# Optimization experiments

Measured on AMD Instinct MI355X. Metric: run time of the kernel, lower is better.

The kernel has to match this reference:

```python
import jax, jax.numpy as jnp
import numpy as np

B, S, E = 4, 2048, 1024
H = 16
D = E // H  # head_dim = 64


def setup_inputs() -> dict:
    key = jax.random.key(0)
    k1, k2, k3 = jax.random.split(key, 3)
    scale_qkv = 1.0 / np.sqrt(E)
    return {
        "x": jax.random.normal(k1, (B, S, E), dtype=jnp.float32),
        "Wqkv": jax.random.normal(k2, (E, 3 * E), dtype=jnp.float32) * scale_qkv,
        "bqkv": jnp.zeros((3 * E,), dtype=jnp.float32),
        "Wproj": jax.random.normal(k3, (E, E), dtype=jnp.float32) * scale_qkv,
        "bproj": jnp.zeros((E,), dtype=jnp.float32),
    }


def reference(x, Wqkv, bqkv, Wproj, bproj):
    b, s, e = x.shape
    qkv = x @ Wqkv + bqkv                      # [B,S,3E]
    q, k, v = jnp.split(qkv, 3, axis=-1)
    # [B,S,E] -> [B,H,S,D]
    q = q.reshape(b, s, H, D).transpose(0, 2, 1, 3)
    k = k.reshape(b, s, H, D).transpose(0, 2, 1, 3)
    v = v.reshape(b, s, H, D).transpose(0, 2, 1, 3)
    scores = jnp.einsum('bhqd,bhkd->bhqk', q, k) * (D ** -0.5)  # [B,H,S,S]
    causal = jnp.tril(jnp.ones((s, s), dtype=bool))
    scores = jnp.where(causal, scores, -jnp.inf)
    weights = jax.nn.softmax(scores, axis=-1)  # dropout p=0 -> identity
    out = jnp.einsum('bhqk,bhkd->bhqd', weights, v)  # [B,H,S,D]
    out = out.transpose(0, 2, 1, 3).reshape(b, s, e)
    return out @ Wproj + bproj
```

## Files before the change

kernel.cpp:

```cpp
#include <hip/hip_runtime.h>
#include <hip/hip_bf16.h>
#include <stdint.h>

#define B_ 4
#define S_ 2048
#define E_ 1024
#define H_ 16
#define D_ 64
#define M_ 8192
#define N1_ 3072
#define QSCALE 0.18033688011112042f

typedef __attribute__((ext_vector_type(8))) short bf16x8;
typedef __attribute__((ext_vector_type(4))) float f32x4;
typedef __attribute__((ext_vector_type(16))) float f32x16;
typedef __attribute__((ext_vector_type(4))) short short4v;

__device__ __forceinline__ short f2b(float f) {
  union { float f; unsigned u; } c; c.f = f;
  unsigned u = c.u + 0x7fffu + ((c.u >> 16) & 1u);
  return (short)(u >> 16);
}

__device__ __forceinline__ float fexp2(float x) {
#if __has_builtin(__builtin_amdgcn_exp2f)
  return __builtin_amdgcn_exp2f(x);
#else
  return exp2f(x);
#endif
}

__device__ __forceinline__ unsigned cvtpk(float lo, float hi2) {
  unsigned r;
  asm("v_cvt_pk_bf16_f32 %0, %1, %2" : "=v"(r) : "v"(lo), "v"(hi2));
  return r;
}

__device__ __forceinline__ void gload16(const void* g, void* l) {
  __builtin_amdgcn_global_load_lds((const __attribute__((address_space(1))) void*)g,
                                   (__attribute__((address_space(3))) void*)l, 16, 0, 0);
}

__global__ void conv_kernel(const float* __restrict__ in, short* __restrict__ out) {
  int idx = blockIdx.x * 256 + threadIdx.x;
  const float4* p = (const float4*)in;
  float4 a = p[(size_t)idx * 2];
  float4 b = p[(size_t)idx * 2 + 1];
  bf16x8 v;
  v[0] = f2b(a.x); v[1] = f2b(a.y); v[2] = f2b(a.z); v[3] = f2b(a.w);
  v[4] = f2b(b.x); v[5] = f2b(b.y); v[6] = f2b(b.z); v[7] = f2b(b.w);
  *(bf16x8*)(out + (size_t)idx * 8) = v;
}

__global__ void trans_kernel(const float* __restrict__ in, short* __restrict__ out,
                             int K, int N) {
  __shared__ float tile[32][33];
  int n0 = blockIdx.x * 32, k0 = blockIdx.y * 32;
  int tx = threadIdx.x & 31, ty = threadIdx.x >> 5;
  #pragma unroll
  for (int i = 0; i < 4; ++i)
    tile[ty + i * 8][tx] = in[(size_t)(k0 + ty + i * 8) * N + n0 + tx];
  __syncthreads();
  #pragma unroll
  for (int i = 0; i < 4; ++i)
    out[(size_t)(n0 + ty + i * 8) * K + k0 + tx] = f2b(tile[tx][ty + i * 8]);
}

template<bool SCATTER>
__global__ __launch_bounds__(256)
void gemm_kernel(const short* __restrict__ A, const short* __restrict__ Bt,
                 const float* __restrict__ bias,
                 short* __restrict__ oQ, short* __restrict__ oK, short* __restrict__ oV,
                 float* __restrict__ oC, int Kdim, int Ndim)
{
  __shared__ short Asub[128 * 64];
  __shared__ short Bsub[128 * 64];
  const int tid = threadIdx.x;
  const int l = tid & 63, w = tid >> 6;
  const int wr = w >> 1, wc = w & 1;
  const int lr = l & 15, lg = l >> 4;

  const int nwg = gridDim.x * gridDim.y;
  const int lin = blockIdx.y * gridDim.x + blockIdx.x;
  const int lin2 = (lin & 7) * (nwg >> 3) + (lin >> 3);
  const int m0 = (lin2 / gridDim.x) * 128, n0 = (lin2 % gridDim.x) * 128;

  const int srow = w * 8 + (l >> 3);
  const int scol = ((l & 7) ^ (l >> 3)) << 3;

  f32x4 acc[4][4] = {};

  for (int k0 = 0; k0 < Kdim; k0 += 64) {
    __syncthreads();
    #pragma unroll
    for (int i = 0; i < 4; ++i) {
      gload16(A  + (size_t)(m0 + i * 32 + srow) * Kdim + k0 + scol,
              (char*)Asub + (i * 32 + w * 8) * 128);
      gload16(Bt + (size_t)(n0 + i * 32 + srow) * Kdim + k0 + scol,
              (char*)Bsub + (i * 32 + w * 8) * 128);
    }
    __syncthreads();
    #pragma unroll
    for (int kk = 0; kk < 64; kk += 32) {
      bf16x8 af[4], bfr[4];
      const int ce2 = (kk + lg * 8) << 1;
      #pragma unroll
      for (int mi = 0; mi < 4; ++mi) {
        int rr = wr * 64 + mi * 16 + lr;
        af[mi] = *(const bf16x8*)((const char*)Asub + rr * 128 + (ce2 ^ ((rr & 7) << 4)));
      }
      #pragma unroll
      for (int ni = 0; ni < 4; ++ni) {
        int rr = wc * 64 + ni * 16 + lr;
        bfr[ni] = *(const bf16x8*)((const char*)Bsub + rr * 128 + (ce2 ^ ((rr & 7) << 4)));
      }
      __builtin_amdgcn_s_setprio(1);
      #pragma unroll
      for (int mi = 0; mi < 4; ++mi)
        #pragma unroll
        for (int ni = 0; ni < 4; ++ni)
          acc[mi][ni] = __builtin_amdgcn_mfma_f32_16x16x32_bf16(af[mi], bfr[ni], acc[mi][ni], 0, 0, 0);
      __builtin_amdgcn_s_setprio(0);
    }
  }

  #pragma unroll
  for (int mi = 0; mi < 4; ++mi) {
    #pragma unroll
    for (int ni = 0; ni < 4; ++ni) {
      const int row0 = m0 + wr * 64 + mi * 16 + lg * 4;
      const int col  = n0 + wc * 64 + ni * 16 + lr;
      const float bv = bias[col];
      if constexpr (SCATTER) {
        const int which = col >> 10;
        const int e = col & 1023;
        const int h = e >> 6, d = e & 63;
        const int b = row0 >> 11, s = row0 & 2047;
        if (which == 2) {
          short4v pv;
          #pragma unroll
          for (int r = 0; r < 4; ++r) pv[r] = f2b(acc[mi][ni][r] + bv);
          *(short4v*)(oV + ((size_t)((b * H_ + h) * D_ + d)) * S_ + s) = pv;
        } else {
          short* dst = which ? oK : oQ;
          const float sc = which ? 1.0f : QSCALE;
          #pragma unroll
          for (int r = 0; r < 4; ++r)
            dst[((size_t)((b * H_ + h) * S_ + s + r)) * D_ + d] = f2b((acc[mi][ni][r] + bv) * sc);
        }
      } else {
        #pragma unroll
        for (int r = 0; r < 4; ++r)
          oC[(size_t)(row0 + r) * Ndim + col] = acc[mi][ni][r] + bv;
      }
    }
  }
}

__global__ __launch_bounds__(512)
void attn_kernel(const short* __restrict__ Q, const short* __restrict__ K,
                 const short* __restrict__ vT, short* __restrict__ O)
{
  __shared__ short Kl[4][64 * 64];
  __shared__ short Vl[4][64 * 64];

  const int qt = (S_ / 128 - 1) - (blockIdx.x >> 6);
  const int bh = blockIdx.x & 63;
  const int tid = threadIdx.x, l = tid & 63, w = tid >> 6;
  const int qw = w & 3, g = w >> 2;
  const int lc = l & 31, hi = l >> 5;
  const int sl8 = l >> 3;
  const int scol = 8 * ((l & 7) ^ sl8);

  const short* Qb = Q  + (size_t)bh * (S_ * D_);
  const short* Kb = K  + (size_t)bh * (S_ * D_);
  const short* Vg = vT + (size_t)bh * (S_ * D_);

  const int q0w = qt * 128 + qw * 32;
  const int ktL = (q0w + 31) >> 6;
  const int NT2 = qt + 1;

  bf16x8 qr[4];
  #pragma unroll
  for (int ds = 0; ds < 4; ++ds)
    qr[ds] = *(const bf16x8*)(Qb + (size_t)(q0w + lc) * D_ + ds * 16 + hi * 8);

  f32x16 accA{}, accB{};
  float lsum = 0.f;

  auto stage = [&](int slot, int kt2) {
    short* kl = &Kl[slot][(qw * 8) * 64];
    short* vl = &Vl[slot][(qw * 8) * 64];
    const size_t kr = (size_t)(kt2 * 64 + qw * 8 + sl8);
    gload16(Kb + kr * 64 + scol, kl);
    gload16(Kb + (kr + 32) * 64 + scol, kl + 32 * 64);
    const size_t vr = (size_t)(qw * 8 + sl8);
    gload16(Vg + vr * S_ + kt2 * 64 + scol, vl);
    gload16(Vg + (vr + 32) * S_ + kt2 * 64 + scol, vl + 32 * 64);
  };

  stage(g * 2, g);
  __syncthreads();

  for (int i = 0; i < NT2; ++i) {
    const int kt = 2 * i + g;
    const int slot = g * 2 + (i & 1);
    if (i + 1 < NT2) stage(g * 2 + ((i & 1) ^ 1), kt + 2);

    if (kt <= ktL) {
      const char* Kc = (const char*)Kl[slot];
      const char* Vc = (const char*)Vl[slot];
      const int rsw = (lc & 7) << 4;
      f32x16 s0{}, s1{};
      __builtin_amdgcn_s_setprio(1);
      #pragma unroll
      for (int ds = 0; ds < 4; ++ds) {
        const int byt = ds * 32 + hi * 16;
        bf16x8 a0 = *(const bf16x8*)(Kc + lc * 128 + (byt ^ rsw));
        bf16x8 a1 = *(const bf16x8*)(Kc + (32 + lc) * 128 + (byt ^ rsw));
        s0 = __builtin_amdgcn_mfma_f32_32x32x16_bf16(a0, qr[ds], s0, 0, 0, 0);
        s1 = __builtin_amdgcn_mfma_f32_32x32x16_bf16(a1, qr[ds], s1, 0, 0, 0);
      }
      __builtin_amdgcn_s_setprio(0);
      float p[32];
      #pragma unroll
      for (int r = 0; r < 16; ++r) { p[r] = s0[r]; p[16 + r] = s1[r]; }
      if (kt == ktL) {
        const int qq = q0w + lc - kt * 64;
        #pragma unroll
        for (int r = 0; r < 16; ++r) {
          const int k0 = (r & 3) + 8 * (r >> 2) + 4 * hi;
          if (k0 > qq)      p[r]      = -1e30f;
          if (k0 + 32 > qq) p[16 + r] = -1e30f;
        }
      }
      float rs0 = 0.f, rs1 = 0.f, rs2 = 0.f, rs3 = 0.f;
      #pragma unroll
      for (int r = 0; r < 8; ++r) {
        p[r]      = fexp2(p[r]);      rs0 += p[r];
        p[8 + r]  = fexp2(p[8 + r]);  rs1 += p[8 + r];
        p[16 + r] = fexp2(p[16 + r]); rs2 += p[16 + r];
        p[24 + r] = fexp2(p[24 + r]); rs3 += p[24 + r];
      }
      float rs = (rs0 + rs1) + (rs2 + rs3);
      rs += __shfl_xor(rs, 32);
      lsum += rs;
      #pragma unroll
      for (int ks = 0; ks < 4; ++ks) {
        const int b8 = ks * 8;
        const unsigned A0 = cvtpk(p[b8 + 0], p[b8 + 1]);
        const unsigned A1 = cvtpk(p[b8 + 2], p[b8 + 3]);
        const unsigned B0 = cvtpk(p[b8 + 4], p[b8 + 5]);
        const unsigned B1 = cvtpk(p[b8 + 6], p[b8 + 7]);
        const unsigned u0 = __shfl_xor(hi ? A0 : B0, 32);
        const unsigned u1 = __shfl_xor(hi ? A1 : B1, 32);
        union { unsigned u[4]; bf16x8 v; } W;
        W.u[0] = hi ? u0 : A0;
        W.u[1] = hi ? u1 : A1;
        W.u[2] = hi ? B0 : u0;
        W.u[3] = hi ? B1 : u1;
        const int byt = ks * 32 + hi * 16;
        bf16x8 va = *(const bf16x8*)(Vc + lc * 128 + (byt ^ rsw));
        bf16x8 vb = *(const bf16x8*)(Vc + (32 + lc) * 128 + (byt ^ rsw));
        __builtin_amdgcn_s_setprio(1);
        accA = __builtin_amdgcn_mfma_f32_32x32x16_bf16(va, W.v, accA, 0, 0, 0);
        accB = __builtin_amdgcn_mfma_f32_32x32x16_bf16(vb, W.v, accB, 0, 0, 0);
        __builtin_amdgcn_s_setprio(0);
      }
    }
    __syncthreads();
  }

  float* accsA = (float*)Kl;
  float* accsB = (float*)Vl;
  float* stats = (float*)((char*)Kl + 20480);
  const int mi = qw * 64 + l;
  if (g == 1) {
    #pragma unroll
    for (int r = 0; r < 16; ++r) {
      accsA[mi * 17 + r] = accA[r];
      accsB[mi * 17 + r] = accB[r];
    }
    stats[mi] = lsum;
  }
  __syncthreads();
  if (g == 0) {
    const float rl = 1.0f / (lsum + stats[mi]);
    const int h = bh & 15, b = bh >> 4;
    short* Ob = O + ((size_t)(b * S_ + q0w + lc)) * E_ + h * 64;
    #pragma unroll
    for (int gq = 0; gq < 4; ++gq) {
      short4v o0, o1;
      #pragma unroll
      for (int i = 0; i < 4; ++i) {
        o0[i] = f2b((accA[4 * gq + i] + accsA[mi * 17 + 4 * gq + i]) * rl);
        o1[i] = f2b((accB[4 * gq + i] + accsB[mi * 17 + 4 * gq + i]) * rl);
      }
      *(short4v*)(Ob + 8 * gq + 4 * hi) = o0;
      *(short4v*)(Ob + 32 + 8 * gq + 4 * hi) = o1;
    }
  }
}

extern "C" void kernel_launch(void* const* d_in, const int* in_sizes, int n_in,
                              void* d_out, int out_size, void* d_ws, size_t ws_size,
                              hipStream_t stream)
{
  const float* x     = (const float*)d_in[0];
  const float* Wqkv  = (const float*)d_in[1];
  const float* bqkv  = (const float*)d_in[2];
  const float* Wproj = (const float*)d_in[3];
  const float* bproj = (const float*)d_in[4];
  float* out = (float*)d_out;

  char* ws = (char*)d_ws;
  short* xb     = (short*)(ws + (size_t)0);
  short* wqkvT  = (short*)(ws + (size_t)16 * 1024 * 1024);
  short* wprojT = (short*)(ws + (size_t)22 * 1024 * 1024);
  short* qb     = (short*)(ws + (size_t)24 * 1024 * 1024);
  short* kb     = (short*)(ws + (size_t)40 * 1024 * 1024);
  short* vb     = (short*)(ws + (size_t)56 * 1024 * 1024);
  short* ob     = (short*)(ws + (size_t)72 * 1024 * 1024);

  conv_kernel<<<4096, 256, 0, stream>>>(x, xb);
  trans_kernel<<<dim3(N1_ / 32, E_ / 32), 256, 0, stream>>>(Wqkv, wqkvT, E_, N1_);
  trans_kernel<<<dim3(E_ / 32, E_ / 32), 256, 0, stream>>>(Wproj, wprojT, E_, E_);
  gemm_kernel<true><<<dim3(N1_ / 128, M_ / 128), 256, 0, stream>>>(
      xb, wqkvT, bqkv, qb, kb, vb, nullptr, E_, N1_);
  attn_kernel<<<(S_ / 128) * (B_ * H_), 512, 0, stream>>>(qb, kb, vb, ob);
  gemm_kernel<false><<<dim3(E_ / 128, M_ / 128), 256, 0, stream>>>(
      ob, wprojT, bproj, nullptr, nullptr, nullptr, out, E_, E_);
}
```

Before: 165.6 us.

## Use 256x128 GEMM tiles with triple-buffered async LDS prefetch

Both GEMM launches now use 512-thread blocks that compute 256x128 output tiles, with each wave owning a 128x32 slab. A three-stage LDS ring filled by async global-to-LDS loads prefetches two K-steps ahead, and a vmcnt wait plus a single barrier per iteration replace the two syncthreads. The goal is to overlap global loads with MFMA work and raise arithmetic intensity per block. In exchange the kernel needs 144KB of dynamic LDS, so only one block fits per CU, and the grid is halved, which may leave CUs underfilled on the smaller projection GEMM.

```diff
diff --git a/kernel.cpp b/kernel.cpp
--- a/kernel.cpp
+++ b/kernel.cpp
@@ -67,69 +67,95 @@
 }
 
 template<bool SCATTER>
-__global__ __launch_bounds__(256)
+__global__ __launch_bounds__(512)
 void gemm_kernel(const short* __restrict__ A, const short* __restrict__ Bt,
                  const float* __restrict__ bias,
                  short* __restrict__ oQ, short* __restrict__ oK, short* __restrict__ oV,
                  float* __restrict__ oC, int Kdim, int Ndim)
 {
-  __shared__ short Asub[128 * 64];
-  __shared__ short Bsub[128 * 64];
+  extern __shared__ char smem[];
+  char* Ab = smem;
+  char* Bb = smem + 3 * 32768;
+
   const int tid = threadIdx.x;
   const int l = tid & 63, w = tid >> 6;
-  const int wr = w >> 1, wc = w & 1;
+  const int wr = w >> 2, wc = w & 3;
   const int lr = l & 15, lg = l >> 4;
 
   const int nwg = gridDim.x * gridDim.y;
   const int lin = blockIdx.y * gridDim.x + blockIdx.x;
   const int lin2 = (lin & 7) * (nwg >> 3) + (lin >> 3);
-  const int m0 = (lin2 / gridDim.x) * 128, n0 = (lin2 % gridDim.x) * 128;
-
-  const int srow = w * 8 + (l >> 3);
-  const int scol = ((l & 7) ^ (l >> 3)) << 3;
-
-  f32x4 acc[4][4] = {};
-
-  for (int k0 = 0; k0 < Kdim; k0 += 64) {
-    __syncthreads();
-    #pragma unroll
-    for (int i = 0; i < 4; ++i) {
-      gload16(A  + (size_t)(m0 + i * 32 + srow) * Kdim + k0 + scol,
-              (char*)Asub + (i * 32 + w * 8) * 128);
-      gload16(Bt + (size_t)(n0 + i * 32 + srow) * Kdim + k0 + scol,
-              (char*)Bsub + (i * 32 + w * 8) * 128);
-    }
-    __syncthreads();
+  const int m0 = (lin2 / gridDim.x) * 256, n0 = (lin2 % gridDim.x) * 128;
+
+  const int srow = tid >> 3;
+  const int scol = 8 * ((tid & 7) ^ (srow & 7));
+  const int NT = Kdim >> 6;
+
+  f32x4 acc[8][2] = {};
+
+  #define STAGE_A(buf, t, chunk) \
+    gload16(A + (size_t)(m0 + (chunk) * 64 + srow) * Kdim + (t) * 64 + scol, \
+            Ab + (buf) * 32768 + (chunk) * 8192 + tid * 16)
+  #define STAGE_B(buf, t, chunk) \
+    gload16(Bt + (size_t)(n0 + (chunk) * 64 + srow) * Kdim + (t) * 64 + scol, \
+            Bb + (buf) * 16384 + (chunk) * 8192 + tid * 16)
+
+  STAGE_A(0, 0, 0); STAGE_A(0, 0, 1); STAGE_A(0, 0, 2); STAGE_A(0, 0, 3);
+  STAGE_B(0, 0, 0); STAGE_B(0, 0, 1);
+  if (NT > 1) {
+    STAGE_A(1, 1, 0); STAGE_A(1, 1, 1); STAGE_A(1, 1, 2); STAGE_A(1, 1, 3);
+    STAGE_B(1, 1, 0); STAGE_B(1, 1, 1);
+  }
+
+  int buf = 0;
+  for (int t = 0; t < NT; ++t) {
+    if (t + 1 < NT) asm volatile("s_waitcnt vmcnt(6)" ::: "memory");
+    else            asm volatile("s_waitcnt vmcnt(0)" ::: "memory");
+    __builtin_amdgcn_s_barrier();
+    asm volatile("" ::: "memory");
+
+    const char* Ac = Ab + buf * 32768;
+    const char* Bc = Bb + buf * 16384;
+    const int nbuf = buf == 0 ? 2 : buf - 1;
+    const bool pf = (t + 2 < NT);
+
     #pragma unroll
     for (int kk = 0; kk < 64; kk += 32) {
-      bf16x8 af[4], bfr[4];
+      bf16x8 af[8], bfr[2];
       const int ce2 = (kk + lg * 8) << 1;
       #pragma unroll
-      for (int mi = 0; mi < 4; ++mi) {
-        int rr = wr * 64 + mi * 16 + lr;
-        af[mi] = *(const bf16x8*)((const char*)Asub + rr * 128 + (ce2 ^ ((rr & 7) << 4)));
-      }
-      #pragma unroll
-      for (int ni = 0; ni < 4; ++ni) {
-        int rr = wc * 64 + ni * 16 + lr;
-        bfr[ni] = *(const bf16x8*)((const char*)Bsub + rr * 128 + (ce2 ^ ((rr & 7) << 4)));
+      for (int mi = 0; mi < 8; ++mi) {
+        int rr = wr * 128 + mi * 16 + lr;
+        af[mi] = *(const bf16x8*)(Ac + rr * 128 + (ce2 ^ ((rr & 7) << 4)));
+      }
+      #pragma unroll
+      for (int ni = 0; ni < 2; ++ni) {
+        int rr = wc * 32 + ni * 16 + lr;
+        bfr[ni] = *(const bf16x8*)(Bc + rr * 128 + (ce2 ^ ((rr & 7) << 4)));
+      }
+      if (pf) {
+        if (kk == 0) { STAGE_A(nbuf, t + 2, 0); STAGE_A(nbuf, t + 2, 1); STAGE_B(nbuf, t + 2, 0); }
+        else         { STAGE_A(nbuf, t + 2, 2); STAGE_A(nbuf, t + 2, 3); STAGE_B(nbuf, t + 2, 1); }
       }
       __builtin_amdgcn_s_setprio(1);
       #pragma unroll
-      for (int mi = 0; mi < 4; ++mi)
+      for (int mi = 0; mi < 8; ++mi)
         #pragma unroll
-        for (int ni = 0; ni < 4; ++ni)
+        for (int ni = 0; ni < 2; ++ni)
           acc[mi][ni] = __builtin_amdgcn_mfma_f32_16x16x32_bf16(af[mi], bfr[ni], acc[mi][ni], 0, 0, 0);
       __builtin_amdgcn_s_setprio(0);
     }
-  }
+    buf = buf == 2 ? 0 : buf + 1;
+  }
+  #undef STAGE_A
+  #undef STAGE_B
 
   #pragma unroll
-  for (int mi = 0; mi < 4; ++mi) {
+  for (int mi = 0; mi < 8; ++mi) {
     #pragma unroll
-    for (int ni = 0; ni < 4; ++ni) {
-      const int row0 = m0 + wr * 64 + mi * 16 + lg * 4;
-      const int col  = n0 + wc * 64 + ni * 16 + lr;
+    for (int ni = 0; ni < 2; ++ni) {
+      const int row0 = m0 + wr * 128 + mi * 16 + lg * 4;
+      const int col  = n0 + wc * 32 + ni * 16 + lr;
       const float bv = bias[col];
       if constexpr (SCATTER) {
         const int which = col >> 10;
@@ -322,12 +348,18 @@
   short* vb     = (short*)(ws + (size_t)56 * 1024 * 1024);
   short* ob     = (short*)(ws + (size_t)72 * 1024 * 1024);
 
+  const int smem_gemm = 3 * 32768 + 3 * 16384;
+  (void)hipFuncSetAttribute(reinterpret_cast<const void*>(gemm_kernel<true>),
+                            hipFuncAttributeMaxDynamicSharedMemorySize, smem_gemm);
+  (void)hipFuncSetAttribute(reinterpret_cast<const void*>(gemm_kernel<false>),
+                            hipFuncAttributeMaxDynamicSharedMemorySize, smem_gemm);
+
   conv_kernel<<<4096, 256, 0, stream>>>(x, xb);
   trans_kernel<<<dim3(N1_ / 32, E_ / 32), 256, 0, stream>>>(Wqkv, wqkvT, E_, N1_);
   trans_kernel<<<dim3(E_ / 32, E_ / 32), 256, 0, stream>>>(Wproj, wprojT, E_, E_);
-  gemm_kernel<true><<<dim3(N1_ / 128, M_ / 128), 256, 0, stream>>>(
+  gemm_kernel<true><<<dim3(N1_ / 128, M_ / 256), 512, smem_gemm, stream>>>(
       xb, wqkvT, bqkv, qb, kb, vb, nullptr, E_, N1_);
   attn_kernel<<<(S_ / 128) * (B_ * H_), 512, 0, stream>>>(qb, kb, vb, ob);
-  gemm_kernel<false><<<dim3(E_ / 128, M_ / 128), 256, 0, stream>>>(
+  gemm_kernel<false><<<dim3(E_ / 128, M_ / 256), 512, smem_gemm, stream>>>(
       ob, wprojT, bproj, nullptr, nullptr, nullptr, out, E_, E_);
 }
```

Measured after the change: 165.2 us. No clear change (-0.3%).

## Rewrite GEMMs with larger tiles and multi-stage async LDS pipeline

Applied to the files above, without the earlier changes.

Replaces the 128x128 single-buffered GEMM with a templated 512-thread kernel using 256x256 (QKV) and 128x256 (proj) tiles and a 5-slot LDS ring. Loads run four K-steps ahead, with vmcnt waits and a single barrier per step. The goal is to overlap global loads with MFMA work and to raise data reuse per workgroup. The cost is much larger dynamic shared memory, which may limit occupancy, and fewer workgroups for the projection GEMM.

```diff
diff --git a/kernel.cpp b/kernel.cpp
--- a/kernel.cpp
+++ b/kernel.cpp
@@ -9,6 +9,7 @@
 #define D_ 64
 #define M_ 8192
 #define N1_ 3072
+#define KD_ 1024
 #define QSCALE 0.18033688011112042f
 
 typedef __attribute__((ext_vector_type(8))) short bf16x8;
@@ -39,6 +40,17 @@
 __device__ __forceinline__ void gload16(const void* g, void* l) {
   __builtin_amdgcn_global_load_lds((const __attribute__((address_space(1))) void*)g,
                                    (__attribute__((address_space(3))) void*)l, 16, 0, 0);
+}
+
+template<int N> __device__ __forceinline__ void wait_vmcnt() {
+  if constexpr (N == 0)       asm volatile("s_waitcnt vmcnt(0)" ::: "memory");
+  else if constexpr (N == 3)  asm volatile("s_waitcnt vmcnt(3)" ::: "memory");
+  else if constexpr (N == 4)  asm volatile("s_waitcnt vmcnt(4)" ::: "memory");
+  else if constexpr (N == 6)  asm volatile("s_waitcnt vmcnt(6)" ::: "memory");
+  else if constexpr (N == 8)  asm volatile("s_waitcnt vmcnt(8)" ::: "memory");
+  else if constexpr (N == 9)  asm volatile("s_waitcnt vmcnt(9)" ::: "memory");
+  else if constexpr (N == 12) asm volatile("s_waitcnt vmcnt(12)" ::: "memory");
+  else static_assert(N == 0, "unsupported vmcnt");
 }
 
 __global__ void conv_kernel(const float* __restrict__ in, short* __restrict__ out) {
@@ -66,87 +78,105 @@
     out[(size_t)(n0 + ty + i * 8) * K + k0 + tx] = f2b(tile[tx][ty + i * 8]);
 }
 
-template<bool SCATTER>
-__global__ __launch_bounds__(256)
-void gemm_kernel(const short* __restrict__ A, const short* __restrict__ Bt,
-                 const float* __restrict__ bias,
-                 short* __restrict__ oQ, short* __restrict__ oK, short* __restrict__ oV,
-                 float* __restrict__ oC, int Kdim, int Ndim)
+template<int MI, int NI, bool SCATTER>
+__global__ __launch_bounds__(512, 2)
+void gemm2(const short* __restrict__ A, const short* __restrict__ Bt,
+           const float* __restrict__ bias,
+           short* __restrict__ oQ, short* __restrict__ oK, short* __restrict__ oV,
+           float* __restrict__ oC, int Ndim)
 {
-  __shared__ short Asub[128 * 64];
-  __shared__ short Bsub[128 * 64];
+  constexpr int BM = MI * 32;
+  constexpr int BN = NI * 64;
+  constexpr int LA = BM / 128;
+  constexpr int LB = BN / 128;
+  constexpr int LH = LA + LB;
+  constexpr int HS = (BM + BN) * 64;
+  constexpr int NH = KD_ / 32;
+
+  extern __shared__ char smem[];
   const int tid = threadIdx.x;
   const int l = tid & 63, w = tid >> 6;
-  const int wr = w >> 1, wc = w & 1;
+  const int wr = w >> 2, wc = w & 3;
   const int lr = l & 15, lg = l >> 4;
 
   const int nwg = gridDim.x * gridDim.y;
   const int lin = blockIdx.y * gridDim.x + blockIdx.x;
   const int lin2 = (lin & 7) * (nwg >> 3) + (lin >> 3);
-  const int m0 = (lin2 / gridDim.x) * 128, n0 = (lin2 % gridDim.x) * 128;
-
-  const int srow = w * 8 + (l >> 3);
-  const int scol = ((l & 7) ^ (l >> 3)) << 3;
-
-  f32x4 acc[4][4] = {};
-
-  for (int k0 = 0; k0 < Kdim; k0 += 64) {
-    __syncthreads();
-    #pragma unroll
-    for (int i = 0; i < 4; ++i) {
-      gload16(A  + (size_t)(m0 + i * 32 + srow) * Kdim + k0 + scol,
-              (char*)Asub + (i * 32 + w * 8) * 128);
-      gload16(Bt + (size_t)(n0 + i * 32 + srow) * Kdim + k0 + scol,
-              (char*)Bsub + (i * 32 + w * 8) * 128);
-    }
-    __syncthreads();
-    #pragma unroll
-    for (int kk = 0; kk < 64; kk += 32) {
-      bf16x8 af[4], bfr[4];
-      const int ce2 = (kk + lg * 8) << 1;
-      #pragma unroll
-      for (int mi = 0; mi < 4; ++mi) {
-        int rr = wr * 64 + mi * 16 + lr;
-        af[mi] = *(const bf16x8*)((const char*)Asub + rr * 128 + (ce2 ^ ((rr & 7) << 4)));
-      }
-      #pragma unroll
-      for (int ni = 0; ni < 4; ++ni) {
-        int rr = wc * 64 + ni * 16 + lr;
-        bfr[ni] = *(const bf16x8*)((const char*)Bsub + rr * 128 + (ce2 ^ ((rr & 7) << 4)));
-      }
-      __builtin_amdgcn_s_setprio(1);
-      #pragma unroll
-      for (int mi = 0; mi < 4; ++mi)
-        #pragma unroll
-        for (int ni = 0; ni < 4; ++ni)
-          acc[mi][ni] = __builtin_amdgcn_mfma_f32_16x16x32_bf16(af[mi], bfr[ni], acc[mi][ni], 0, 0, 0);
-      __builtin_amdgcn_s_setprio(0);
-    }
+  const int m0 = (lin2 / gridDim.x) * BM, n0 = (lin2 % gridDim.x) * BN;
+
+  const int srow = tid >> 2;
+  const int sc8 = 8 * ((tid & 3) ^ ((tid >> 3) & 3));
+
+  f32x4 acc[MI][NI] = {};
+
+  auto stage = [&](int h) {
+    char* base = smem + (h % 5) * HS;
+    #pragma unroll
+    for (int i = 0; i < LA; ++i)
+      gload16(A + (size_t)(m0 + i * 128 + srow) * KD_ + h * 32 + sc8,
+              base + i * 8192 + tid * 16);
+    #pragma unroll
+    for (int i = 0; i < LB; ++i)
+      gload16(Bt + (size_t)(n0 + i * 128 + srow) * KD_ + h * 32 + sc8,
+              base + BM * 64 + i * 8192 + tid * 16);
+  };
+
+  stage(0); stage(1); stage(2); stage(3);
+
+  for (int h = 0; h < NH; ++h) {
+    if (h <= NH - 4)      wait_vmcnt<3 * LH>();
+    else if (h == NH - 3) wait_vmcnt<2 * LH>();
+    else if (h == NH - 2) wait_vmcnt<LH>();
+    else                  wait_vmcnt<0>();
+    __builtin_amdgcn_s_barrier();
+    asm volatile("" ::: "memory");
+    if (h + 4 < NH) stage(h + 4);
+
+    const char* Ac = smem + (h % 5) * HS;
+    const char* Bc = Ac + BM * 64;
+    bf16x8 af[MI], bfr[NI];
+    #pragma unroll
+    for (int mi = 0; mi < MI; ++mi) {
+      const int rr = wr * (MI * 16) + mi * 16 + lr;
+      af[mi] = *(const bf16x8*)(Ac + rr * 64 + ((lg ^ ((rr >> 1) & 3)) << 4));
+    }
+    #pragma unroll
+    for (int ni = 0; ni < NI; ++ni) {
+      const int rr = wc * (NI * 16) + ni * 16 + lr;
+      bfr[ni] = *(const bf16x8*)(Bc + rr * 64 + ((lg ^ ((rr >> 1) & 3)) << 4));
+    }
+    __builtin_amdgcn_s_setprio(1);
+    #pragma unroll
+    for (int mi = 0; mi < MI; ++mi)
+      #pragma unroll
+      for (int ni = 0; ni < NI; ++ni)
+        acc[mi][ni] = __builtin_amdgcn_mfma_f32_16x16x32_bf16(af[mi], bfr[ni], acc[mi][ni], 0, 0, 0);
+    __builtin_amdgcn_s_setprio(0);
   }
 
   #pragma unroll
-  for (int mi = 0; mi < 4; ++mi) {
-    #pragma unroll
-    for (int ni = 0; ni < 4; ++ni) {
-      const int row0 = m0 + wr * 64 + mi * 16 + lg * 4;
-      const int col  = n0 + wc * 64 + ni * 16 + lr;
+  for (int mi = 0; mi < MI; ++mi) {
+    #pragma unroll
+    for (int ni = 0; ni < NI; ++ni) {
+      const int row0 = m0 + wr * (MI * 16) + mi * 16 + lg * 4;
+      const int col  = n0 + wc * (NI * 16) + ni * 16 + lr;
       const float bv = bias[col];
       if constexpr (SCATTER) {
         const int which = col >> 10;
         const int e = col & 1023;
-        const int h = e >> 6, d = e & 63;
+        const int h2 = e >> 6, d = e & 63;
         const int b = row0 >> 11, s = row0 & 2047;
         if (which == 2) {
           short4v pv;
           #pragma unroll
           for (int r = 0; r < 4; ++r) pv[r] = f2b(acc[mi][ni][r] + bv);
-          *(short4v*)(oV + ((size_t)((b * H_ + h) * D_ + d)) * S_ + s) = pv;
+          *(short4v*)(oV + ((size_t)((b * H_ + h2) * D_ + d)) * S_ + s) = pv;
         } else {
           short* dst = which ? oK : oQ;
           const float sc = which ? 1.0f : QSCALE;
           #pragma unroll
           for (int r = 0; r < 4; ++r)
-            dst[((size_t)((b * H_ + h) * S_ + s + r)) * D_ + d] = f2b((acc[mi][ni][r] + bv) * sc);
+            dst[((size_t)((b * H_ + h2) * S_ + s + r)) * D_ + d] = f2b((acc[mi][ni][r] + bv) * sc);
         }
       } else {
         #pragma unroll
@@ -322,12 +352,19 @@
   short* vb     = (short*)(ws + (size_t)56 * 1024 * 1024);
   short* ob     = (short*)(ws + (size_t)72 * 1024 * 1024);
 
+  const int smem_qkv  = (256 + 256) * 64 * 5;
+  const int smem_proj = (128 + 256) * 64 * 5;
+  (void)hipFuncSetAttribute(reinterpret_cast<const void*>(gemm2<8, 4, true>),
+                            hipFuncAttributeMaxDynamicSharedMemorySize, smem_qkv);
+  (void)hipFuncSetAttribute(reinterpret_cast<const void*>(gemm2<4, 4, false>),
+                            hipFuncAttributeMaxDynamicSharedMemorySize, smem_proj);
+
   conv_kernel<<<4096, 256, 0, stream>>>(x, xb);
   trans_kernel<<<dim3(N1_ / 32, E_ / 32), 256, 0, stream>>>(Wqkv, wqkvT, E_, N1_);
   trans_kernel<<<dim3(E_ / 32, E_ / 32), 256, 0, stream>>>(Wproj, wprojT, E_, E_);
-  gemm_kernel<true><<<dim3(N1_ / 128, M_ / 128), 256, 0, stream>>>(
-      xb, wqkvT, bqkv, qb, kb, vb, nullptr, E_, N1_);
+  gemm2<8, 4, true><<<dim3(N1_ / 256, M_ / 256), 512, smem_qkv, stream>>>(
+      xb, wqkvT, bqkv, qb, kb, vb, nullptr, N1_);
   attn_kernel<<<(S_ / 128) * (B_ * H_), 512, 0, stream>>>(qb, kb, vb, ob);
-  gemm_kernel<false><<<dim3(E_ / 128, M_ / 128), 256, 0, stream>>>(
-      ob, wprojT, bproj, nullptr, nullptr, nullptr, out, E_, E_);
-}
+  gemm2<4, 4, false><<<dim3(E_ / 256, M_ / 128), 512, smem_proj, stream>>>(
+      ob, wprojT, bproj, nullptr, nullptr, nullptr, out, E_);
+}
```

After: 167.6 us. About the same (+1.2%).

## Software-pipeline attention: defer PV MFMA one tile to overlap with softmax

Applied to the files above, without the earlier changes.

Restructures the attention inner loop so the P·V matrix multiply for the previous key tile runs right after the current tile's QK^T, overlapping MFMA work with the exp/softmax ALU work of the current tile. Probabilities are kept packed in registers across iterations. V staging moves to a triple buffer so the deferred tile stays resident while new tiles load, and a drain step runs after the loop. Costs extra registers (16 packed words) and more shared memory, which may lower occupancy.

```diff
diff --git a/kernel.cpp b/kernel.cpp
--- a/kernel.cpp
+++ b/kernel.cpp
@@ -161,8 +161,8 @@
 void attn_kernel(const short* __restrict__ Q, const short* __restrict__ K,
                  const short* __restrict__ vT, short* __restrict__ O)
 {
-  __shared__ short Kl[4][64 * 64];
-  __shared__ short Vl[4][64 * 64];
+  __shared__ short Kl[2][2][64 * 64];
+  __shared__ short Vl[2][3][64 * 64];
 
   const int qt = (S_ / 128 - 1) - (blockIdx.x >> 6);
   const int bh = blockIdx.x & 63;
@@ -187,10 +187,11 @@
 
   f32x16 accA{}, accB{};
   float lsum = 0.f;
-
-  auto stage = [&](int slot, int kt2) {
-    short* kl = &Kl[slot][(qw * 8) * 64];
-    short* vl = &Vl[slot][(qw * 8) * 64];
+  const int rsw = (lc & 7) << 4;
+
+  auto stage = [&](int ks_, int vs_, int kt2) {
+    short* kl = &Kl[g][ks_][(qw * 8) * 64];
+    short* vl = &Vl[g][vs_][(qw * 8) * 64];
     const size_t kr = (size_t)(kt2 * 64 + qw * 8 + sl8);
     gload16(Kb + kr * 64 + scol, kl);
     gload16(Kb + (kr + 32) * 64 + scol, kl + 32 * 64);
@@ -199,19 +200,22 @@
     gload16(Vg + (vr + 32) * S_ + kt2 * 64 + scol, vl + 32 * 64);
   };
 
-  stage(g * 2, g);
+  stage(0, 0, g);
   __syncthreads();
+
+  unsigned pw[16];
+  #pragma unroll
+  for (int z = 0; z < 16; ++z) pw[z] = 0u;
+  bool havePrev = false;
 
   for (int i = 0; i < NT2; ++i) {
     const int kt = 2 * i + g;
-    const int slot = g * 2 + (i & 1);
-    if (i + 1 < NT2) stage(g * 2 + ((i & 1) ^ 1), kt + 2);
-
-    if (kt <= ktL) {
-      const char* Kc = (const char*)Kl[slot];
-      const char* Vc = (const char*)Vl[slot];
-      const int rsw = (lc & 7) << 4;
-      f32x16 s0{}, s1{};
+    if (i + 1 < NT2) stage((i + 1) & 1, (i + 1) % 3, kt + 2);
+
+    const bool active = (kt <= ktL);
+    f32x16 s0{}, s1{};
+    if (active) {
+      const char* Kc = (const char*)Kl[g][i & 1];
       __builtin_amdgcn_s_setprio(1);
       #pragma unroll
       for (int ds = 0; ds < 4; ++ds) {
@@ -222,6 +226,24 @@
         s1 = __builtin_amdgcn_mfma_f32_32x32x16_bf16(a1, qr[ds], s1, 0, 0, 0);
       }
       __builtin_amdgcn_s_setprio(0);
+    }
+    if (havePrev) {
+      const char* Vc = (const char*)Vl[g][(i + 2) % 3];
+      __builtin_amdgcn_s_setprio(1);
+      #pragma unroll
+      for (int ks = 0; ks < 4; ++ks) {
+        union { unsigned u[4]; bf16x8 v; } W;
+        W.u[0] = pw[ks * 4 + 0]; W.u[1] = pw[ks * 4 + 1];
+        W.u[2] = pw[ks * 4 + 2]; W.u[3] = pw[ks * 4 + 3];
+        const int byt = ks * 32 + hi * 16;
+        bf16x8 va = *(const bf16x8*)(Vc + lc * 128 + (byt ^ rsw));
+        bf16x8 vb = *(const bf16x8*)(Vc + (32 + lc) * 128 + (byt ^ rsw));
+        accA = __builtin_amdgcn_mfma_f32_32x32x16_bf16(va, W.v, accA, 0, 0, 0);
+        accB = __builtin_amdgcn_mfma_f32_32x32x16_bf16(vb, W.v, accB, 0, 0, 0);
+      }
+      __builtin_amdgcn_s_setprio(0);
+    }
+    if (active) {
       float p[32];
       #pragma unroll
       for (int r = 0; r < 16; ++r) { p[r] = s0[r]; p[16 + r] = s1[r]; }
@@ -254,22 +276,33 @@
         const unsigned B1 = cvtpk(p[b8 + 6], p[b8 + 7]);
         const unsigned u0 = __shfl_xor(hi ? A0 : B0, 32);
         const unsigned u1 = __shfl_xor(hi ? A1 : B1, 32);
-        union { unsigned u[4]; bf16x8 v; } W;
-        W.u[0] = hi ? u0 : A0;
-        W.u[1] = hi ? u1 : A1;
-        W.u[2] = hi ? B0 : u0;
-        W.u[3] = hi ? B1 : u1;
-        const int byt = ks * 32 + hi * 16;
-        bf16x8 va = *(const bf16x8*)(Vc + lc * 128 + (byt ^ rsw));
-        bf16x8 vb = *(const bf16x8*)(Vc + (32 + lc) * 128 + (byt ^ rsw));
-        __builtin_amdgcn_s_setprio(1);
-        accA = __builtin_amdgcn_mfma_f32_32x32x16_bf16(va, W.v, accA, 0, 0, 0);
-        accB = __builtin_amdgcn_mfma_f32_32x32x16_bf16(vb, W.v, accB, 0, 0, 0);
-        __builtin_amdgcn_s_setprio(0);
-      }
+        pw[ks * 4 + 0] = hi ? u0 : A0;
+        pw[ks * 4 + 1] = hi ? u1 : A1;
+        pw[ks * 4 + 2] = hi ? B0 : u0;
+        pw[ks * 4 + 3] = hi ? B1 : u1;
+      }
+      havePrev = true;
+    } else {
+      havePrev = false;
     }
     __syncthreads();
   }
+
+  if (havePrev) {
+    const char* Vc = (const char*)Vl[g][(NT2 - 1) % 3];
+    #pragma unroll
+    for (int ks = 0; ks < 4; ++ks) {
+      union { unsigned u[4]; bf16x8 v; } W;
+      W.u[0] = pw[ks * 4 + 0]; W.u[1] = pw[ks * 4 + 1];
+      W.u[2] = pw[ks * 4 + 2]; W.u[3] = pw[ks * 4 + 3];
+      const int byt = ks * 32 + hi * 16;
+      bf16x8 va = *(const bf16x8*)(Vc + lc * 128 + (byt ^ rsw));
+      bf16x8 vb = *(const bf16x8*)(Vc + (32 + lc) * 128 + (byt ^ rsw));
+      accA = __builtin_amdgcn_mfma_f32_32x32x16_bf16(va, W.v, accA, 0, 0, 0);
+      accB = __builtin_amdgcn_mfma_f32_32x32x16_bf16(vb, W.v, accB, 0, 0, 0);
+    }
+  }
+  __syncthreads();
 
   float* accsA = (float*)Kl;
   float* accsB = (float*)Vl;
```

Result: slower. 182.4 us (+10.1%).
